# Performance work log

Measured on AMD Instinct MI355X. Metric: run time of the kernel, lower is better.

## Reference

```python
import jax, jax.numpy as jnp
import numpy as np

VOCABSIZE = 100000
EMBEDSIZE = 128
BATCH = 262144


def setup_inputs() -> dict:
    key = jax.random.key(0)
    k1, k2, k3, k4, k5 = jax.random.split(key, 5)
    xs = jax.random.randint(k1, (BATCH,), 0, VOCABSIZE, dtype=jnp.int64 if jax.config.jax_enable_x64 else jnp.int32)
    ys = jax.random.randint(k2, (BATCH,), 0, VOCABSIZE, dtype=jnp.int64 if jax.config.jax_enable_x64 else jnp.int32)
    metric = jax.random.normal(k3, (EMBEDSIZE, EMBEDSIZE), dtype=jnp.float32)
    EMBEDM = jax.random.normal(k4, (VOCABSIZE, EMBEDSIZE), dtype=jnp.float32)
    # Original inits NEGEMBEDM to zeros; we use small random values so the
    # output / gradients are non-degenerate for kernel correctness testing.
    NEGEMBEDM = jax.random.normal(k5, (VOCABSIZE, EMBEDSIZE), dtype=jnp.float32) * 0.1
    return {"xs": xs, "ys": ys, "metric": metric, "EMBEDM": EMBEDM, "NEGEMBEDM": NEGEMBEDM}


def reference(xs, ys, metric, EMBEDM, NEGEMBEDM):
    # Faithful math: diag((E[xs] @ metric) @ N[ys].T) == sum((E[xs] @ metric) * N[ys], -1).
    # We compute the batched bilinear form directly, avoiding the O(B^2*D)
    # full matmul + diag extraction of the original.
    xsembeds = EMBEDM[xs]          # [B, D]
    ysembeds = NEGEMBEDM[ys]       # [B, D]
    d = jnp.einsum('bd,de,be->b', xsembeds, metric, ysembeds)  # [B]
    return jax.nn.sigmoid(2.0 * d - 1.0)
```

## Files before the change

### kernel.cpp

```cpp
#include <hip/hip_runtime.h>
#include <hip/hip_fp16.h>

#define D      128
#define NROWS  100000
#define RB     64
#define NE     ((NROWS + RB - 1) / RB)
#define NN     (NROWS / 16)
#define NPREP  (NE + NN)

typedef __attribute__((ext_vector_type(8))) _Float16 f16x8;
typedef __attribute__((ext_vector_type(2))) _Float16 f16x2;
typedef __attribute__((ext_vector_type(4))) float    f32x4;

union F16x8U { _Float16 h[8]; f16x8 v; };
union F32x4U { float f[4]; f32x4 v; };

typedef __attribute__((address_space(1))) const void gvoid;
typedef __attribute__((address_space(3))) void       lvoid;

__global__ __launch_bounds__(256) void convert_M16(
    const float* __restrict__ M,
    _Float16* __restrict__ mh, _Float16* __restrict__ ml)
{
    const int q    = blockIdx.x * 256 + threadIdx.x;
    const int kk   = q >> 9;
    const int cf   = (q >> 6) & 7;
    const int lane = q & 63;
    const int col  = cf * 16 + (lane & 15);
    const int k0   = kk * 32 + (lane >> 4) * 8;

    F16x8U h, l;
    #pragma unroll
    for (int j = 0; j < 8; ++j) {
        float f = M[(k0 + j) * D + col];
        _Float16 hh = (_Float16)f;
        h.h[j] = hh;
        l.h[j] = (_Float16)(f - (float)hh);
    }
    *(f16x8*)(mh + q * 8) = h.v;
    *(f16x8*)(ml + q * 8) = l.v;
}

__global__ __launch_bounds__(256, 3) void fused_prep4(
    const float* __restrict__ E, const float* __restrict__ N,
    const _Float16* __restrict__ mh, const _Float16* __restrict__ ml,
    _Float16* __restrict__ Ep, _Float16* __restrict__ Np)
{
    __shared__ float lds[RB * D];

    const int tid = threadIdx.x;
    const int bid = (int)blockIdx.x;

    if (bid % 5 != 0) {
        const int nid = bid - bid / 5 - 1;
        const int l16 = tid & 15;
        const int row = nid * 16 + (tid >> 4);
        const float* src = N + (size_t)row * D + l16;
        F16x8U o;
        #pragma unroll
        for (int k = 0; k < 8; ++k) o.h[k] = (_Float16)src[16 * k];
        *(f16x8*)(Np + (size_t)row * D + l16 * 8) = o.v;
        return;
    }

    const int eid  = bid / 5;
    const int lane = tid & 63;
    const int w    = tid >> 6;
    const int rb   = eid * RB;
    const int lrow = lane & 15;
    const int lk   = lane >> 4;

    #pragma unroll
    for (int i = 0; i < 8; ++i) {
        const int S  = w * 512 + i * 64 + lane;
        const int r  = S >> 5;
        const int u  = (S & 31) ^ (r & 15);
        const int gr = min(rb + r, NROWS - 1);
        const float* src = E + (size_t)gr * D + u * 4;
        __builtin_amdgcn_global_load_lds(
            (gvoid*)src, (lvoid*)&lds[(w * 512 + i * 64) * 4], 16, 0, 0);
    }

    f16x8 bh[4][2], bl[4][2];
    #pragma unroll
    for (int kk = 0; kk < 4; ++kk)
        #pragma unroll
        for (int cfl = 0; cfl < 2; ++cfl) {
            const int off = ((kk * 8 + w * 2 + cfl) * 64 + lane) * 8;
            bh[kk][cfl] = *(const f16x8*)(mh + off);
            bl[kk][cfl] = *(const f16x8*)(ml + off);
        }

    f32x4 acc[4][2];
    #pragma unroll
    for (int rf = 0; rf < 4; ++rf)
        #pragma unroll
        for (int cfl = 0; cfl < 2; ++cfl)
            acc[rf][cfl] = (f32x4){0.f, 0.f, 0.f, 0.f};

    asm volatile("s_waitcnt vmcnt(0)" ::: "memory");
    __syncthreads();
    __builtin_amdgcn_sched_barrier(0);

    #pragma unroll
    for (int kk = 0; kk < 4; ++kk) {
        F16x8U a16[4];
        #pragma unroll
        for (int rf = 0; rf < 4; ++rf) {
            const int r  = rf * 16 + lrow;
            const int t0 = kk * 8 + lk * 2;
            F32x4U x, y;
            x.v = *(const f32x4*)&lds[(r * 32 + ((t0    ) ^ (r & 15))) * 4];
            y.v = *(const f32x4*)&lds[(r * 32 + ((t0 + 1) ^ (r & 15))) * 4];
            #pragma unroll
            for (int j = 0; j < 4; ++j) {
                a16[rf].h[j]     = (_Float16)x.f[j];
                a16[rf].h[j + 4] = (_Float16)y.f[j];
            }
        }

        #pragma unroll
        for (int rf = 0; rf < 4; ++rf)
            #pragma unroll
            for (int cfl = 0; cfl < 2; ++cfl) {
                acc[rf][cfl] = __builtin_amdgcn_mfma_f32_16x16x32_f16(
                    a16[rf].v, bh[kk][cfl], acc[rf][cfl], 0, 0, 0);
                acc[rf][cfl] = __builtin_amdgcn_mfma_f32_16x16x32_f16(
                    a16[rf].v, bl[kk][cfl], acc[rf][cfl], 0, 0, 0);
            }
    }

    #pragma unroll
    for (int rf = 0; rf < 4; ++rf)
        #pragma unroll
        for (int i = 0; i < 4; ++i) {
            const int row = rb + rf * 16 + lk * 4 + i;
            if (row < NROWS) {
                f16x2 o;
                o[0] = (_Float16)acc[rf][0][i];
                o[1] = (_Float16)acc[rf][1][i];
                *(f16x2*)(Ep + (size_t)row * D + lrow * 8 + w * 2) = o;
            }
        }
}

__global__ __launch_bounds__(256) void gather_dot16(
    const int* __restrict__ xs, const int* __restrict__ ys,
    const _Float16* __restrict__ Ep, const _Float16* __restrict__ Np,
    float* __restrict__ out)
{
    const int tid = threadIdx.x;
    const int o0  = blockIdx.x * 32 + (tid >> 4) * 2;
    const int l   = tid & 15;

    const int x0 = xs[o0], x1 = xs[o0 + 1];
    const int y0 = ys[o0], y1 = ys[o0 + 1];

    const f16x8 a0 = *(const f16x8*)(Ep + (size_t)x0 * D + l * 8);
    const f16x8 b0 = *(const f16x8*)(Np + (size_t)y0 * D + l * 8);
    const f16x8 a1 = *(const f16x8*)(Ep + (size_t)x1 * D + l * 8);
    const f16x8 b1 = *(const f16x8*)(Np + (size_t)y1 * D + l * 8);

    float r0 = 0.f, r1 = 0.f;
    #pragma unroll
    for (int j = 0; j < 8; ++j) {
        r0 += (float)a0[j] * (float)b0[j];
        r1 += (float)a1[j] * (float)b1[j];
    }

    r0 += __shfl_xor(r0, 1); r1 += __shfl_xor(r1, 1);
    r0 += __shfl_xor(r0, 2); r1 += __shfl_xor(r1, 2);
    r0 += __shfl_xor(r0, 4); r1 += __shfl_xor(r1, 4);
    r0 += __shfl_xor(r0, 8); r1 += __shfl_xor(r1, 8);

    if (l == 0) {
        float2 v;
        v.x = 1.0f / (1.0f + __expf(1.0f - 2.0f * r0));
        v.y = 1.0f / (1.0f + __expf(1.0f - 2.0f * r1));
        *(float2*)(out + o0) = v;
    }
}

extern "C" void kernel_launch(void* const* d_in, const int* in_sizes, int n_in,
                              void* d_out, int out_size, void* d_ws, size_t ws_size,
                              hipStream_t stream) {
    const int*   xs     = (const int*)d_in[0];
    const int*   ys     = (const int*)d_in[1];
    const float* metric = (const float*)d_in[2];
    const float* EMBEDM = (const float*)d_in[3];
    const float* NEGEM  = (const float*)d_in[4];
    float*       out    = (float*)d_out;

    const int B = in_sizes[0];

    char* ws = (char*)d_ws;
    _Float16* Ep = (_Float16*)ws;
    _Float16* Np = (_Float16*)(ws + (32u << 20));
    _Float16* mh = (_Float16*)(ws + (64u << 20));
    _Float16* ml = (_Float16*)(ws + (64u << 20) + (64u << 10));

    convert_M16<<<8, 256, 0, stream>>>(metric, mh, ml);

    fused_prep4<<<NPREP, 256, 0, stream>>>(EMBEDM, NEGEM, mh, ml, Ep, Np);

    gather_dot16<<<B / 32, 256, 0, stream>>>(xs, ys, Ep, Np, out);
}
```

Before: 55.38 us.

## Drop NEGEMBEDM fp16 conversion pass and gather fp32 rows directly in dot kernel

Removes the pass that converted all of NEGEMBEDM to fp16, which read 51MB and wrote 25MB. The dot kernel now gathers fp32 rows of N directly using a strided per-lane layout that matches the permuted Ep column ordering. The prep kernel becomes a pure E@M GEMM, and its metric fragment loads are hoisted ahead of the LDS loads. The trade is that the gather now reads twice as many bytes per N row, with 4-byte strided loads instead of 16-byte vector loads.

```diff
diff --git a/kernel.cpp b/kernel.cpp
--- a/kernel.cpp
+++ b/kernel.cpp
@@ -5,8 +5,6 @@
 #define NROWS  100000
 #define RB     64
 #define NE     ((NROWS + RB - 1) / RB)
-#define NN     (NROWS / 16)
-#define NPREP  (NE + NN)
 
 typedef __attribute__((ext_vector_type(8))) _Float16 f16x8;
 typedef __attribute__((ext_vector_type(2))) _Float16 f16x2;
@@ -41,34 +39,29 @@
     *(f16x8*)(ml + q * 8) = l.v;
 }
 
-__global__ __launch_bounds__(256, 3) void fused_prep4(
-    const float* __restrict__ E, const float* __restrict__ N,
+__global__ __launch_bounds__(256, 3) void gemm_E(
+    const float* __restrict__ E,
     const _Float16* __restrict__ mh, const _Float16* __restrict__ ml,
-    _Float16* __restrict__ Ep, _Float16* __restrict__ Np)
+    _Float16* __restrict__ Ep)
 {
     __shared__ float lds[RB * D];
 
-    const int tid = threadIdx.x;
-    const int bid = (int)blockIdx.x;
-
-    if (bid % 5 != 0) {
-        const int nid = bid - bid / 5 - 1;
-        const int l16 = tid & 15;
-        const int row = nid * 16 + (tid >> 4);
-        const float* src = N + (size_t)row * D + l16;
-        F16x8U o;
-        #pragma unroll
-        for (int k = 0; k < 8; ++k) o.h[k] = (_Float16)src[16 * k];
-        *(f16x8*)(Np + (size_t)row * D + l16 * 8) = o.v;
-        return;
-    }
-
-    const int eid  = bid / 5;
+    const int tid  = threadIdx.x;
     const int lane = tid & 63;
     const int w    = tid >> 6;
-    const int rb   = eid * RB;
+    const int rb   = (int)blockIdx.x * RB;
     const int lrow = lane & 15;
     const int lk   = lane >> 4;
+
+    f16x8 bh[4][2], bl[4][2];
+    #pragma unroll
+    for (int kk = 0; kk < 4; ++kk)
+        #pragma unroll
+        for (int cfl = 0; cfl < 2; ++cfl) {
+            const int off = ((kk * 8 + w * 2 + cfl) * 64 + lane) * 8;
+            bh[kk][cfl] = *(const f16x8*)(mh + off);
+            bl[kk][cfl] = *(const f16x8*)(ml + off);
+        }
 
     #pragma unroll
     for (int i = 0; i < 8; ++i) {
@@ -81,16 +74,6 @@
             (gvoid*)src, (lvoid*)&lds[(w * 512 + i * 64) * 4], 16, 0, 0);
     }
 
-    f16x8 bh[4][2], bl[4][2];
-    #pragma unroll
-    for (int kk = 0; kk < 4; ++kk)
-        #pragma unroll
-        for (int cfl = 0; cfl < 2; ++cfl) {
-            const int off = ((kk * 8 + w * 2 + cfl) * 64 + lane) * 8;
-            bh[kk][cfl] = *(const f16x8*)(mh + off);
-            bl[kk][cfl] = *(const f16x8*)(ml + off);
-        }
-
     f32x4 acc[4][2];
     #pragma unroll
     for (int rf = 0; rf < 4; ++rf)
@@ -101,6 +84,12 @@
     asm volatile("s_waitcnt vmcnt(0)" ::: "memory");
     __syncthreads();
     __builtin_amdgcn_sched_barrier(0);
+
+    #pragma unroll
+    for (int kk = 0; kk < 4; ++kk)
+        #pragma unroll
+        for (int cfl = 0; cfl < 2; ++cfl)
+            asm volatile("" : "+v"(bh[kk][cfl]), "+v"(bl[kk][cfl]));
 
     #pragma unroll
     for (int kk = 0; kk < 4; ++kk) {
@@ -144,9 +133,9 @@
         }
 }
 
-__global__ __launch_bounds__(256) void gather_dot16(
+__global__ __launch_bounds__(256) void gather_dotN(
     const int* __restrict__ xs, const int* __restrict__ ys,
-    const _Float16* __restrict__ Ep, const _Float16* __restrict__ Np,
+    const _Float16* __restrict__ Ep, const float* __restrict__ N,
     float* __restrict__ out)
 {
     const int tid = threadIdx.x;
@@ -157,15 +146,15 @@
     const int y0 = ys[o0], y1 = ys[o0 + 1];
 
     const f16x8 a0 = *(const f16x8*)(Ep + (size_t)x0 * D + l * 8);
-    const f16x8 b0 = *(const f16x8*)(Np + (size_t)y0 * D + l * 8);
     const f16x8 a1 = *(const f16x8*)(Ep + (size_t)x1 * D + l * 8);
-    const f16x8 b1 = *(const f16x8*)(Np + (size_t)y1 * D + l * 8);
+    const float* n0 = N + (size_t)y0 * D + l;
+    const float* n1 = N + (size_t)y1 * D + l;
 
     float r0 = 0.f, r1 = 0.f;
     #pragma unroll
     for (int j = 0; j < 8; ++j) {
-        r0 += (float)a0[j] * (float)b0[j];
-        r1 += (float)a1[j] * (float)b1[j];
+        r0 += (float)a0[j] * n0[16 * j];
+        r1 += (float)a1[j] * n1[16 * j];
     }
 
     r0 += __shfl_xor(r0, 1); r1 += __shfl_xor(r1, 1);
@@ -195,13 +184,12 @@
 
     char* ws = (char*)d_ws;
     _Float16* Ep = (_Float16*)ws;
-    _Float16* Np = (_Float16*)(ws + (32u << 20));
     _Float16* mh = (_Float16*)(ws + (64u << 20));
     _Float16* ml = (_Float16*)(ws + (64u << 20) + (64u << 10));
 
     convert_M16<<<8, 256, 0, stream>>>(metric, mh, ml);
 
-    fused_prep4<<<NPREP, 256, 0, stream>>>(EMBEDM, NEGEM, mh, ml, Ep, Np);
+    gemm_E<<<NE, 256, 0, stream>>>(EMBEDM, mh, ml, Ep);
 
-    gather_dot16<<<B / 32, 256, 0, stream>>>(xs, ys, Ep, Np, out);
+    gather_dotN<<<B / 32, 256, 0, stream>>>(xs, ys, Ep, NEGEM, out);
 }
```

Measured after the change: 56.88 us. 1.03x slower.
